# Kernel tuning notes

Hardware: AMD Instinct MI355X
Metric: run time of the kernel (lower is better)

The kernel has to match this reference:

```python
import jax, jax.numpy as jnp
import numpy as np

B, C, Wd, Ht = 16, 256, 64, 64
C2 = C // 2

def setup_inputs() -> dict:
    key = jax.random.key(0)
    ks = jax.random.split(key, 9)
    s = 0.05  # keep logits in a sane range (d_qk=128)
    return {
        "x": jax.random.normal(ks[0], (B, C, Wd, Ht), jnp.float32),
        "y": jax.random.normal(ks[1], (B, C, Wd, Ht), jnp.float32),
        "Wq": jax.random.normal(ks[2], (C2, C), jnp.float32) * s,
        "bq": jax.random.normal(ks[3], (C2,), jnp.float32) * s,
        "Wk": jax.random.normal(ks[4], (C2, C), jnp.float32) * s,
        "bk": jax.random.normal(ks[5], (C2,), jnp.float32) * s,
        "Wv": jax.random.normal(ks[6], (C, C), jnp.float32) * s,
        "bv": jax.random.normal(ks[7], (C,), jnp.float32) * s,
        "gamma": jax.random.normal(ks[8], (1,), jnp.float32),
    }

def reference(x, y, Wq, bq, Wk, bk, Wv, bv, gamma):
    b, c, w, h = x.shape
    n = w * h
    xf = x.reshape(b, c, n)           # (B, C, N)
    yf = y.reshape(b, c, n)           # (B, C, N)
    # conv1x1 == channel matmul
    q = jnp.einsum('oc,bcn->bno', Wq, xf) + bq                    # (B, N, C2)
    k = jnp.einsum('oc,bcn->bon', Wk, yf) + bk[None, :, None]     # (B, C2, N)
    energy = jnp.einsum('bno,bom->bnm', q, k)                     # (B, N, N)
    attn = jax.nn.softmax(energy, axis=-1)
    v = jnp.einsum('oc,bcn->bon', Wv, yf) + bv[None, :, None]     # (B, C, N)
    out = jnp.einsum('bon,bmn->bom', v, attn)                     # V @ attn^T
    out = out.reshape(b, c, w, h)
    return gamma[0] * out + y
```

## Files before the change

kernel.cpp:

```cpp
#include <hip/hip_runtime.h>
#include <stdint.h>

using f32x4  = __attribute__((ext_vector_type(4))) float;
using f32x16 = __attribute__((ext_vector_type(16))) float;
using f16x8  = __attribute__((ext_vector_type(8))) _Float16;

#define NB  16
#define NC  256
#define NC2 128
#define NN  4096
#define TILE_B 49152
#define LOG2E 1.44269504f

__device__ __forceinline__ unsigned int pk2(float a, float b) {
    auto h = __builtin_amdgcn_cvt_pkrtz(a, b);
    return __builtin_bit_cast(unsigned int, h);
}

__device__ __forceinline__ f16x8 pack8(f32x4 a, f32x4 b) {
    union { unsigned int w[4]; f16x8 v; } u;
    u.w[0] = pk2(a[0], a[1]); u.w[1] = pk2(a[2], a[3]);
    u.w[2] = pk2(b[0], b[1]); u.w[3] = pk2(b[2], b[3]);
    return u.v;
}

__device__ __forceinline__ void gload16(const void* g, void* l) {
    __builtin_amdgcn_global_load_lds(
        (const __attribute__((address_space(1))) unsigned int*)g,
        (__attribute__((address_space(3))) unsigned int*)l, 16, 0, 0);
}

__global__ __launch_bounds__(256, 2) void qkv_kernel(
    const float* __restrict__ x, const float* __restrict__ y,
    const float* __restrict__ Wq, const float* __restrict__ bq,
    const float* __restrict__ Wk, const float* __restrict__ bk,
    const float* __restrict__ Wv, const float* __restrict__ bv,
    unsigned short* __restrict__ Qf, char* __restrict__ KV)
{
    __shared__ __align__(16) char lds[65536];

    const int bid   = blockIdx.x;
    const int ntile = bid & 63;
    const int bb    = bid >> 6;
    const int nblk  = ntile * 64;

    const int t    = threadIdx.x;
    const int lane = t & 63;
    const int wid  = t >> 6;
    const int l31  = lane & 31;
    const int s    = lane >> 5;

    {
        const bool isQ = (wid < 2);
        const float* srcb = (isQ ? x : y) + (size_t)bb * NC * NN;
        const float* W    = isQ ? Wq : Wk;
        const float* bias = isQ ? bq : bk;
        const int wo = (wid & 1) * 64;
        const int base = isQ ? 49152 : 0;
        const float osc = isQ ? LOG2E : 1.0f;

        f32x16 acc[2][2];
        #pragma unroll
        for (int a = 0; a < 2; ++a)
            #pragma unroll
            for (int bc = 0; bc < 2; ++bc) acc[a][bc] = (f32x16)(0.0f);

        #pragma unroll 4
        for (int ks = 0; ks < 16; ++ks) {
            const int c0 = ks * 16 + s * 8;
            f16x8 wf[2], xf[2];
            #pragma unroll
            for (int a = 0; a < 2; ++a) {
                const float* wr = W + (size_t)(wo + a * 32 + l31) * NC + c0;
                wf[a] = pack8(*(const f32x4*)wr, *(const f32x4*)(wr + 4));
            }
            #pragma unroll
            for (int bc = 0; bc < 2; ++bc) {
                const float* xc = srcb + (size_t)c0 * NN + nblk + bc * 32 + l31;
                f32x4 v0, v1;
                v0[0] = xc[0*NN]; v0[1] = xc[1*NN]; v0[2] = xc[2*NN]; v0[3] = xc[3*NN];
                v1[0] = xc[4*NN]; v1[1] = xc[5*NN]; v1[2] = xc[6*NN]; v1[3] = xc[7*NN];
                xf[bc] = pack8(v0, v1);
            }
            #pragma unroll
            for (int a = 0; a < 2; ++a)
                #pragma unroll
                for (int bc = 0; bc < 2; ++bc)
                    acc[a][bc] = __builtin_amdgcn_mfma_f32_32x32x16_f16(
                        wf[a], xf[bc], acc[a][bc], 0, 0, 0);
        }

        #pragma unroll
        for (int a = 0; a < 2; ++a) {
            #pragma unroll
            for (int bc = 0; bc < 2; ++bc) {
                const int nr = bc * 32 + l31;
                #pragma unroll
                for (int g = 0; g < 4; ++g) {
                    const int o0 = wo + a * 32 + 8 * g + 4 * s;
                    const f32x4 bv4 = *(const f32x4*)(bias + o0);
                    union { unsigned int w[2]; uint2 u2; } pk;
                    pk.w[0] = pk2((acc[a][bc][g*4+0] + bv4[0]) * osc,
                                  (acc[a][bc][g*4+1] + bv4[1]) * osc);
                    pk.w[1] = pk2((acc[a][bc][g*4+2] + bv4[2]) * osc,
                                  (acc[a][bc][g*4+3] + bv4[3]) * osc);
                    const int dst = base + nr*256 +
                        (((o0 >> 3) << 4) ^ ((nr & 15) << 4)) + (o0 & 7) * 2;
                    *(uint2*)(lds + dst) = pk.u2;
                }
            }
        }
    }

    {
        const float* srcb = y + (size_t)bb * NC * NN;
        const int wo = wid * 64;

        f32x16 acc[2][2];
        #pragma unroll
        for (int a = 0; a < 2; ++a)
            #pragma unroll
            for (int bc = 0; bc < 2; ++bc) acc[a][bc] = (f32x16)(0.0f);

        #pragma unroll 4
        for (int ks = 0; ks < 16; ++ks) {
            const int c0 = ks * 16 + s * 8;
            f16x8 wf[2], xf[2];
            #pragma unroll
            for (int a = 0; a < 2; ++a) {
                const float* wr = Wv + (size_t)(wo + a * 32 + l31) * NC + c0;
                wf[a] = pack8(*(const f32x4*)wr, *(const f32x4*)(wr + 4));
            }
            #pragma unroll
            for (int bc = 0; bc < 2; ++bc) {
                const float* xc = srcb + (size_t)c0 * NN + nblk + bc * 32 + l31;
                f32x4 v0, v1;
                v0[0] = xc[0*NN]; v0[1] = xc[1*NN]; v0[2] = xc[2*NN]; v0[3] = xc[3*NN];
                v1[0] = xc[4*NN]; v1[1] = xc[5*NN]; v1[2] = xc[6*NN]; v1[3] = xc[7*NN];
                xf[bc] = pack8(v0, v1);
            }
            #pragma unroll
            for (int a = 0; a < 2; ++a)
                #pragma unroll
                for (int bc = 0; bc < 2; ++bc)
                    acc[a][bc] = __builtin_amdgcn_mfma_f32_32x32x16_f16(
                        xf[bc], wf[a], acc[a][bc], 0, 0, 0);
        }

        #pragma unroll
        for (int a = 0; a < 2; ++a) {
            const int o = wo + a * 32 + l31;
            const float bvo = bv[o];
            #pragma unroll
            for (int bc = 0; bc < 2; ++bc) {
                #pragma unroll
                for (int g = 0; g < 4; ++g) {
                    const int nr = bc * 32 + 8 * g + 4 * s;
                    union { unsigned int w[2]; uint2 u2; } pk;
                    pk.w[0] = pk2(acc[a][bc][g*4+0] + bvo, acc[a][bc][g*4+1] + bvo);
                    pk.w[1] = pk2(acc[a][bc][g*4+2] + bvo, acc[a][bc][g*4+3] + bvo);
                    const int dst = 16384 + ((nr >> 3) << 12) + o*16 + (nr & 7) * 2;
                    *(uint2*)(lds + dst) = pk.u2;
                }
            }
        }
    }

    __syncthreads();

    char* kvt = KV + (size_t)(bb*64 + ntile) * TILE_B;
    #pragma unroll
    for (int i = 0; i < 12; ++i) {
        const int off = (i*256 + t) * 16;
        *(uint4*)(kvt + off) = *(const uint4*)(lds + off);
    }
    char* qg = (char*)Qf + ((size_t)(bb*NN + nblk)) * NC2 * 2;
    #pragma unroll
    for (int i = 0; i < 4; ++i) {
        const int g = (i*256 + t) * 16;
        const int sidx = 49152 + (g ^ (((g >> 8) & 15) << 4));
        *(uint4*)(qg + g) = *(const uint4*)(lds + sidx);
    }
}

__global__ __launch_bounds__(256, 2) void attn_kernel(
    const unsigned short* __restrict__ Qf, const char* __restrict__ KV,
    const float* __restrict__ yg, const float* __restrict__ gamma,
    float* __restrict__ outp)
{
    __shared__ __align__(16) char kls[2][16384];
    __shared__ __align__(16) char vls[32768];

    const int bid = ((blockIdx.x & 7) << 6) + (blockIdx.x >> 3);
    const int bb = bid >> 5;
    const int m0 = (bid & 31) * 128;
    const int t    = threadIdx.x;
    const int lane = t & 63;
    const int wv   = t >> 6;
    const int qcol = lane & 31;
    const int s    = lane >> 5;

    f16x8 qf[8];
    {
        const char* qrow = (const char*)Qf +
            (((size_t)bb*NN + m0 + wv*32 + qcol) * NC2) * 2;
        #pragma unroll
        for (int ks = 0; ks < 8; ++ks)
            qf[ks] = *(const f16x8*)(qrow + ks*32 + s*16);
    }

    f32x16 acc[8];
    #pragma unroll
    for (int ob = 0; ob < 8; ++ob) acc[ob] = (f32x16)(0.0f);
    float m_run = -3.0e38f, l_run = 0.0f;

    const char* kvb = KV + (size_t)bb * 64 * TILE_B;

    #pragma unroll
    for (int i = 0; i < 4; ++i)
        gload16(kvb + ((i*256 + t) << 4), kls[0] + ((i*256 + wv*64) << 4));
    #pragma unroll
    for (int i = 0; i < 8; ++i)
        gload16(kvb + 16384 + ((i*256 + t) << 4), vls + ((i*256 + wv*64) << 4));

    #pragma unroll 1
    for (int it = 0; it < 64; ++it) {
        asm volatile("s_waitcnt vmcnt(8)" ::: "memory");
        __builtin_amdgcn_s_barrier();
        asm volatile("" ::: "memory");

        const char* kbuf = kls[it & 1];
        const char* nsrc = kvb + (size_t)((it + 1) & 63) * TILE_B;

        f32x16 sA = (f32x16)(0.0f), sB = (f32x16)(0.0f);
        {
            const int keyA = qcol, keyB = 32 + qcol;
            const int rbA = keyA * 256, rbB = keyB * 256;
            const int swA = (keyA & 15) << 4, swB = (keyB & 15) << 4;
            __builtin_amdgcn_s_setprio(1);
            #pragma unroll
            for (int ks = 0; ks < 8; ++ks) {
                f16x8 kf = *(const f16x8*)(kbuf + rbA + ((ks*32 + s*16) ^ swA));
                sA = __builtin_amdgcn_mfma_f32_32x32x16_f16(kf, qf[ks], sA, 0, 0, 0);
            }
            #pragma unroll
            for (int ks = 0; ks < 8; ++ks) {
                f16x8 kf = *(const f16x8*)(kbuf + rbB + ((ks*32 + s*16) ^ swB));
                sB = __builtin_amdgcn_mfma_f32_32x32x16_f16(kf, qf[ks], sB, 0, 0, 0);
            }
            __builtin_amdgcn_s_setprio(0);
        }

        {
            char* kdst = (char*)kls[(it + 1) & 1];
            #pragma unroll
            for (int i = 0; i < 4; ++i)
                gload16(nsrc + ((i*256 + t) << 4), kdst + ((i*256 + wv*64) << 4));
        }

        asm volatile("s_waitcnt vmcnt(4)" ::: "memory");
        __builtin_amdgcn_s_barrier();
        asm volatile("" ::: "memory");

        float pa[16], pb[16];
        {
            float mx[16];
            #pragma unroll
            for (int r = 0; r < 16; ++r) mx[r] = fmaxf(sA[r], sB[r]);
            #pragma unroll
            for (int st = 8; st >= 1; st >>= 1)
                #pragma unroll
                for (int r = 0; r < st; ++r) mx[r] = fmaxf(mx[r], mx[r + st]);
            float pmax = fmaxf(mx[0], __shfl_xor(mx[0], 32));
            if (__any(pmax > m_run + 11.5415603f)) {
                const float mn = fmaxf(m_run, pmax);
                const float sc = __builtin_amdgcn_exp2f(m_run - mn);
                m_run = mn; l_run *= sc;
                #pragma unroll
                for (int ob = 0; ob < 8; ++ob)
                    #pragma unroll
                    for (int r = 0; r < 16; ++r) acc[ob][r] *= sc;
            }
            #pragma unroll
            for (int r = 0; r < 16; ++r) pa[r] = __builtin_amdgcn_exp2f(sA[r] - m_run);
            #pragma unroll
            for (int r = 0; r < 16; ++r) pb[r] = __builtin_amdgcn_exp2f(sB[r] - m_run);
            float sm[16];
            #pragma unroll
            for (int r = 0; r < 16; ++r) sm[r] = pa[r] + pb[r];
            #pragma unroll
            for (int st = 8; st >= 1; st >>= 1)
                #pragma unroll
                for (int r = 0; r < st; ++r) sm[r] += sm[r + st];
            l_run += sm[0] + __shfl_xor(sm[0], 32);
        }

        #pragma unroll
        for (int kb = 0; kb < 2; ++kb) {
            const float* pp = kb ? pb : pa;
            f16x8 pfr[2];
            #pragma unroll
            for (int ks2 = 0; ks2 < 2; ++ks2) {
                unsigned int pA0, pA1, pB0, pB1;
                if (ks2 == 0) {
                    pA0 = pk2(pp[0], pp[1]);  pA1 = pk2(pp[2], pp[3]);
                    pB0 = pk2(pp[4], pp[5]);  pB1 = pk2(pp[6], pp[7]);
                } else {
                    pA0 = pk2(pp[8], pp[9]);  pA1 = pk2(pp[10], pp[11]);
                    pB0 = pk2(pp[12], pp[13]); pB1 = pk2(pp[14], pp[15]);
                }
                const unsigned int lv0 = s ? pB0 : pA0;
                const unsigned int lv1 = s ? pB1 : pA1;
                const unsigned int sd0 = s ? pA0 : pB0;
                const unsigned int sd1 = s ? pA1 : pB1;
                const unsigned int rv0 = (unsigned int)__shfl_xor((int)sd0, 32);
                const unsigned int rv1 = (unsigned int)__shfl_xor((int)sd1, 32);
                union { unsigned int w[4]; f16x8 v; } u;
                u.w[0] = s ? rv0 : lv0;
                u.w[1] = s ? rv1 : lv1;
                u.w[2] = s ? lv0 : rv0;
                u.w[3] = s ? lv1 : rv1;
                pfr[ks2] = u.v;
            }
            #pragma unroll
            for (int ks2 = 0; ks2 < 2; ++ks2) {
                const char* vplane = vls + (((kb<<2) + (ks2<<1) + s) << 12) + qcol*16;
                const f16x8 pbx = pfr[ks2];
                __builtin_amdgcn_s_setprio(1);
                #pragma unroll
                for (int ob = 0; ob < 8; ++ob) {
                    f16x8 vf = *(const f16x8*)(vplane + ob*512);
                    acc[ob] = __builtin_amdgcn_mfma_f32_32x32x16_f16(vf, pbx, acc[ob], 0, 0, 0);
                }
                __builtin_amdgcn_s_setprio(0);
            }
        }

        asm volatile("" ::: "memory");
        __builtin_amdgcn_s_barrier();
        asm volatile("" ::: "memory");

        #pragma unroll
        for (int i = 0; i < 8; ++i)
            gload16(nsrc + 16384 + ((i*256 + t) << 4), vls + ((i*256 + wv*64) << 4));
    }
    asm volatile("s_waitcnt vmcnt(0)" ::: "memory");

    const float ga   = gamma[0];
    const float invl = 1.0f / l_run;
    const int n = m0 + wv*32 + qcol;
    #pragma unroll
    for (int ob = 0; ob < 8; ++ob) {
        #pragma unroll
        for (int r = 0; r < 16; ++r) {
            const int o = ob*32 + (r&3) + 8*(r>>2) + 4*s;
            const size_t a = ((size_t)(bb*NC + o))*NN + n;
            outp[a] = fmaf(acc[ob][r]*invl, ga, yg[a]);
        }
    }
}

extern "C" void kernel_launch(void* const* d_in, const int* in_sizes, int n_in,
                              void* d_out, int out_size, void* d_ws, size_t ws_size,
                              hipStream_t stream) {
    (void)in_sizes; (void)n_in; (void)out_size; (void)ws_size;
    const float* x     = (const float*)d_in[0];
    const float* y     = (const float*)d_in[1];
    const float* Wq    = (const float*)d_in[2];
    const float* bq    = (const float*)d_in[3];
    const float* Wk    = (const float*)d_in[4];
    const float* bk    = (const float*)d_in[5];
    const float* Wv    = (const float*)d_in[6];
    const float* bv    = (const float*)d_in[7];
    const float* gamma = (const float*)d_in[8];
    float* out = (float*)d_out;

    unsigned short* Qf = (unsigned short*)d_ws;
    char* KV = (char*)(Qf + (size_t)NB*NN*NC2);

    qkv_kernel<<<dim3(1024), dim3(256), 0, stream>>>(
        x, y, Wq, bq, Wk, bk, Wv, bv, Qf, KV);
    attn_kernel<<<dim3(512), dim3(256), 0, stream>>>(
        Qf, KV, y, gamma, out);
}
```

Before: 303.9 us.

## Reschedule K prefetch and barriers in flash-attention loop, interleave QK MFMAs

The next K tile's global-to-LDS prefetch now starts at the top of each iteration instead of after the QK MFMAs. The V-ready wait and barrier move after the softmax, so the softmax overlaps the outstanding V loads. The separate top-of-loop barrier is folded into a single end-of-iteration vmcnt(0)+barrier, leaving two barriers per iteration instead of three. The two QK MFMA chains are interleaved to hide MFMA dependency latency, and the PV loop is flattened. The trade-off is that the end-of-iteration full vmcnt wait may stall if the K prefetch has not completed.

```diff
diff --git a/kernel.cpp b/kernel.cpp
--- a/kernel.cpp
+++ b/kernel.cpp
@@ -222,15 +222,21 @@
     #pragma unroll
     for (int i = 0; i < 8; ++i)
         gload16(kvb + 16384 + ((i*256 + t) << 4), vls + ((i*256 + wv*64) << 4));
+    asm volatile("s_waitcnt vmcnt(8)" ::: "memory");
+    __builtin_amdgcn_s_barrier();
+    asm volatile("" ::: "memory");
 
     #pragma unroll 1
     for (int it = 0; it < 64; ++it) {
-        asm volatile("s_waitcnt vmcnt(8)" ::: "memory");
-        __builtin_amdgcn_s_barrier();
-        asm volatile("" ::: "memory");
-
         const char* kbuf = kls[it & 1];
         const char* nsrc = kvb + (size_t)((it + 1) & 63) * TILE_B;
+
+        {
+            char* kdst = (char*)kls[(it + 1) & 1];
+            #pragma unroll
+            for (int i = 0; i < 4; ++i)
+                gload16(nsrc + ((i*256 + t) << 4), kdst + ((i*256 + wv*64) << 4));
+        }
 
         f32x16 sA = (f32x16)(0.0f), sB = (f32x16)(0.0f);
         {
@@ -240,27 +246,13 @@
             __builtin_amdgcn_s_setprio(1);
             #pragma unroll
             for (int ks = 0; ks < 8; ++ks) {
-                f16x8 kf = *(const f16x8*)(kbuf + rbA + ((ks*32 + s*16) ^ swA));
-                sA = __builtin_amdgcn_mfma_f32_32x32x16_f16(kf, qf[ks], sA, 0, 0, 0);
-            }
-            #pragma unroll
-            for (int ks = 0; ks < 8; ++ks) {
-                f16x8 kf = *(const f16x8*)(kbuf + rbB + ((ks*32 + s*16) ^ swB));
-                sB = __builtin_amdgcn_mfma_f32_32x32x16_f16(kf, qf[ks], sB, 0, 0, 0);
+                f16x8 kfA = *(const f16x8*)(kbuf + rbA + ((ks*32 + s*16) ^ swA));
+                f16x8 kfB = *(const f16x8*)(kbuf + rbB + ((ks*32 + s*16) ^ swB));
+                sA = __builtin_amdgcn_mfma_f32_32x32x16_f16(kfA, qf[ks], sA, 0, 0, 0);
+                sB = __builtin_amdgcn_mfma_f32_32x32x16_f16(kfB, qf[ks], sB, 0, 0, 0);
             }
             __builtin_amdgcn_s_setprio(0);
         }
-
-        {
-            char* kdst = (char*)kls[(it + 1) & 1];
-            #pragma unroll
-            for (int i = 0; i < 4; ++i)
-                gload16(nsrc + ((i*256 + t) << 4), kdst + ((i*256 + wv*64) << 4));
-        }
-
-        asm volatile("s_waitcnt vmcnt(4)" ::: "memory");
-        __builtin_amdgcn_s_barrier();
-        asm volatile("" ::: "memory");
 
         float pa[16], pb[16];
         {
@@ -295,48 +287,43 @@
             l_run += sm[0] + __shfl_xor(sm[0], 32);
         }
 
-        #pragma unroll
-        for (int kb = 0; kb < 2; ++kb) {
+        asm volatile("s_waitcnt vmcnt(4)" ::: "memory");
+        __builtin_amdgcn_s_barrier();
+        asm volatile("" ::: "memory");
+
+        #pragma unroll
+        for (int st4 = 0; st4 < 4; ++st4) {
+            const int kb  = st4 >> 1;
+            const int ks2 = st4 & 1;
             const float* pp = kb ? pb : pa;
-            f16x8 pfr[2];
-            #pragma unroll
-            for (int ks2 = 0; ks2 < 2; ++ks2) {
-                unsigned int pA0, pA1, pB0, pB1;
-                if (ks2 == 0) {
-                    pA0 = pk2(pp[0], pp[1]);  pA1 = pk2(pp[2], pp[3]);
-                    pB0 = pk2(pp[4], pp[5]);  pB1 = pk2(pp[6], pp[7]);
-                } else {
-                    pA0 = pk2(pp[8], pp[9]);  pA1 = pk2(pp[10], pp[11]);
-                    pB0 = pk2(pp[12], pp[13]); pB1 = pk2(pp[14], pp[15]);
-                }
-                const unsigned int lv0 = s ? pB0 : pA0;
-                const unsigned int lv1 = s ? pB1 : pA1;
-                const unsigned int sd0 = s ? pA0 : pB0;
-                const unsigned int sd1 = s ? pA1 : pB1;
-                const unsigned int rv0 = (unsigned int)__shfl_xor((int)sd0, 32);
-                const unsigned int rv1 = (unsigned int)__shfl_xor((int)sd1, 32);
-                union { unsigned int w[4]; f16x8 v; } u;
-                u.w[0] = s ? rv0 : lv0;
-                u.w[1] = s ? rv1 : lv1;
-                u.w[2] = s ? lv0 : rv0;
-                u.w[3] = s ? lv1 : rv1;
-                pfr[ks2] = u.v;
-            }
-            #pragma unroll
-            for (int ks2 = 0; ks2 < 2; ++ks2) {
-                const char* vplane = vls + (((kb<<2) + (ks2<<1) + s) << 12) + qcol*16;
-                const f16x8 pbx = pfr[ks2];
-                __builtin_amdgcn_s_setprio(1);
-                #pragma unroll
-                for (int ob = 0; ob < 8; ++ob) {
-                    f16x8 vf = *(const f16x8*)(vplane + ob*512);
-                    acc[ob] = __builtin_amdgcn_mfma_f32_32x32x16_f16(vf, pbx, acc[ob], 0, 0, 0);
-                }
-                __builtin_amdgcn_s_setprio(0);
-            }
-        }
-
-        asm volatile("" ::: "memory");
+            const int b0 = ks2 * 8;
+            unsigned int pA0 = pk2(pp[b0+0], pp[b0+1]);
+            unsigned int pA1 = pk2(pp[b0+2], pp[b0+3]);
+            unsigned int pB0 = pk2(pp[b0+4], pp[b0+5]);
+            unsigned int pB1 = pk2(pp[b0+6], pp[b0+7]);
+            const unsigned int lv0 = s ? pB0 : pA0;
+            const unsigned int lv1 = s ? pB1 : pA1;
+            const unsigned int sd0 = s ? pA0 : pB0;
+            const unsigned int sd1 = s ? pA1 : pB1;
+            const unsigned int rv0 = (unsigned int)__shfl_xor((int)sd0, 32);
+            const unsigned int rv1 = (unsigned int)__shfl_xor((int)sd1, 32);
+            union { unsigned int w[4]; f16x8 v; } u;
+            u.w[0] = s ? rv0 : lv0;
+            u.w[1] = s ? rv1 : lv1;
+            u.w[2] = s ? lv0 : rv0;
+            u.w[3] = s ? lv1 : rv1;
+            const f16x8 pbx = u.v;
+            const char* vplane = vls + (((kb<<2) + (ks2<<1) + s) << 12) + qcol*16;
+            __builtin_amdgcn_s_setprio(1);
+            #pragma unroll
+            for (int ob = 0; ob < 8; ++ob) {
+                f16x8 vf = *(const f16x8*)(vplane + ob*512);
+                acc[ob] = __builtin_amdgcn_mfma_f32_32x32x16_f16(vf, pbx, acc[ob], 0, 0, 0);
+            }
+            __builtin_amdgcn_s_setprio(0);
+        }
+
+        asm volatile("s_waitcnt vmcnt(0)" ::: "memory");
         __builtin_amdgcn_s_barrier();
         asm volatile("" ::: "memory");
 
```

Measured after the change: 309.6 us. No clear change (+1.9%).
